# Performance work log

Measured on AMD Instinct MI355X. Metric: run time of the kernel, lower is better.

Reference implementation:

```python
import jax, jax.numpy as jnp
import numpy as np

B, D, CROSS = 16384, 2048, 3

def setup_inputs() -> dict:
    key = jax.random.key(0)
    k1, k2 = jax.random.split(key)
    x = jax.random.normal(k1, (B, D), dtype=jnp.float32)
    # glorot_normal for (d,1) weight ~ std sqrt(2/(d+1))
    W = jax.random.normal(k2, (CROSS, D), dtype=jnp.float32) * np.sqrt(2.0 / (D + 1)).astype(np.float32)
    b = jnp.zeros((CROSS, D), dtype=jnp.float32)
    return {"x": x, "W": W, "b": b}

def reference(x, W, b):
    # Original: xl <- (x0 @ xl^T) @ w_i + b_i + xl  with x0, xl shaped [B,d,1].
    # (x0 xl^T) w == x0 * (xl . w), a scalar per row — mathematically identical,
    # avoiding the wasted [B,d,d] outer product.
    x0 = x
    xl = x
    for i in range(CROSS):
        s = jnp.einsum('bd,d->b', xl, W[i])          # [B] scalar dot per row
        xl = x0 * s[:, None] + b[i][None, :] + xl     # scale + bias + residual
    return xl
```

## Files before the change

### kernel.cpp

```cpp
#include <hip/hip_runtime.h>


constexpr int D_DIM    = 2048;
constexpr int NTHREADS = 256;
constexpr int ROWS     = 2;

__device__ __forceinline__ float dot8(const float4 a0, const float4 a1,
                                      const float4 b0, const float4 b1) {
    return a0.x*b0.x + a0.y*b0.y + a0.z*b0.z + a0.w*b0.w
         + a1.x*b1.x + a1.y*b1.y + a1.z*b1.z + a1.w*b1.w;
}

__global__ __launch_bounds__(NTHREADS)
void cross_network_kernel(const float* __restrict__ x,
                          const float* __restrict__ W,
                          const float* __restrict__ bias,
                          float* __restrict__ out) {
    const int row0 = blockIdx.x * ROWS;
    const int t    = threadIdx.x;
    const int lane = t & 63;
    const int wave = t >> 6;

    const float4* xr0 = reinterpret_cast<const float4*>(x + (size_t)row0 * D_DIM);
    const float4* xr1 = reinterpret_cast<const float4*>(x + (size_t)(row0 + 1) * D_DIM);
    const float4 x0a = xr0[t], x0b = xr0[t + NTHREADS];
    const float4 x1a = xr1[t], x1b = xr1[t + NTHREADS];

    const float4* w0r = reinterpret_cast<const float4*>(W);
    const float4* w1r = reinterpret_cast<const float4*>(W + D_DIM);
    const float4* w2r = reinterpret_cast<const float4*>(W + 2 * D_DIM);
    const float4* b0r = reinterpret_cast<const float4*>(bias);
    const float4* b1r = reinterpret_cast<const float4*>(bias + D_DIM);
    const float4* b2r = reinterpret_cast<const float4*>(bias + 2 * D_DIM);

    float p00, p01, p10, p11, p20, p21, q1, q2;
    float4 bsa, bsb;
    {
        const float4 wa = w0r[t], wb = w0r[t + NTHREADS];
        p00 = dot8(x0a, x0b, wa, wb);
        p01 = dot8(x1a, x1b, wa, wb);
    }
    {
        const float4 wa = w1r[t], wb = w1r[t + NTHREADS];
        p10 = dot8(x0a, x0b, wa, wb);
        p11 = dot8(x1a, x1b, wa, wb);
        bsa = b0r[t]; bsb = b0r[t + NTHREADS];
        q1  = dot8(bsa, bsb, wa, wb);
    }
    {
        const float4 wa = w2r[t], wb = w2r[t + NTHREADS];
        p20 = dot8(x0a, x0b, wa, wb);
        p21 = dot8(x1a, x1b, wa, wb);
        const float4 b1a = b1r[t], b1b = b1r[t + NTHREADS];
        bsa.x += b1a.x; bsa.y += b1a.y; bsa.z += b1a.z; bsa.w += b1a.w;
        bsb.x += b1b.x; bsb.y += b1b.y; bsb.z += b1b.z; bsb.w += b1b.w;
        q2  = dot8(bsa, bsb, wa, wb);
    }

#pragma unroll
    for (int off = 32; off >= 1; off >>= 1) {
        p00 += __shfl_down(p00, off, 64);
        p01 += __shfl_down(p01, off, 64);
        p10 += __shfl_down(p10, off, 64);
        p11 += __shfl_down(p11, off, 64);
        p20 += __shfl_down(p20, off, 64);
        p21 += __shfl_down(p21, off, 64);
        q1  += __shfl_down(q1,  off, 64);
        q2  += __shfl_down(q2,  off, 64);
    }

    __shared__ float sred[8][4];
    if (lane == 0) {
        sred[0][wave] = p00; sred[1][wave] = p01;
        sred[2][wave] = p10; sred[3][wave] = p11;
        sred[4][wave] = p20; sred[5][wave] = p21;
        sred[6][wave] = q1;  sred[7][wave] = q2;
    }
    __syncthreads();

    float d[8];
#pragma unroll
    for (int k = 0; k < 8; ++k)
        d[k] = sred[k][0] + sred[k][1] + sred[k][2] + sred[k][3];
    const float c01 = d[6], c02 = d[7];

    float scale[ROWS];
#pragma unroll
    for (int r = 0; r < ROWS; ++r) {
        const float s0 = d[0 + r];
        const float t1 = 1.0f + s0;
        const float s1 = fmaf(t1, d[2 + r], c01);
        const float t2 = t1 + s1;
        const float s2 = fmaf(t2, d[4 + r], c02);
        scale[r] = t2 + s2;
    }

    {
        const float4 b2a = b2r[t], b2b = b2r[t + NTHREADS];
        bsa.x += b2a.x; bsa.y += b2a.y; bsa.z += b2a.z; bsa.w += b2a.w;
        bsb.x += b2b.x; bsb.y += b2b.y; bsb.z += b2b.z; bsb.w += b2b.w;
    }

    float4* o0 = reinterpret_cast<float4*>(out + (size_t)row0 * D_DIM);
    float4* o1 = reinterpret_cast<float4*>(out + (size_t)(row0 + 1) * D_DIM);
    float4 v;
    v.x = fmaf(x0a.x, scale[0], bsa.x); v.y = fmaf(x0a.y, scale[0], bsa.y);
    v.z = fmaf(x0a.z, scale[0], bsa.z); v.w = fmaf(x0a.w, scale[0], bsa.w);
    o0[t] = v;
    v.x = fmaf(x0b.x, scale[0], bsb.x); v.y = fmaf(x0b.y, scale[0], bsb.y);
    v.z = fmaf(x0b.z, scale[0], bsb.z); v.w = fmaf(x0b.w, scale[0], bsb.w);
    o0[t + NTHREADS] = v;
    v.x = fmaf(x1a.x, scale[1], bsa.x); v.y = fmaf(x1a.y, scale[1], bsa.y);
    v.z = fmaf(x1a.z, scale[1], bsa.z); v.w = fmaf(x1a.w, scale[1], bsa.w);
    o1[t] = v;
    v.x = fmaf(x1b.x, scale[1], bsb.x); v.y = fmaf(x1b.y, scale[1], bsb.y);
    v.z = fmaf(x1b.z, scale[1], bsb.z); v.w = fmaf(x1b.w, scale[1], bsb.w);
    o1[t + NTHREADS] = v;
}

extern "C" void kernel_launch(void* const* d_in, const int* in_sizes, int n_in,
                              void* d_out, int out_size, void* d_ws, size_t ws_size,
                              hipStream_t stream) {
    const float* x    = (const float*)d_in[0];
    const float* W    = (const float*)d_in[1];
    const float* bias = (const float*)d_in[2];
    float* out = (float*)d_out;

    const int B = in_sizes[0] / D_DIM;
    cross_network_kernel<<<B / ROWS, NTHREADS, 0, stream>>>(x, W, bias, out);
}
```

Measured before the change: 43.56 us.

## Process multiple row pairs per block, reusing W and bias sums across rows

Each block now loops over four row pairs, loading W rows and computing the bias-sum vector and bias-W dot constants once, then reusing them from registers and shared memory. This removes redundant W/bias loads and reductions per row pair and cuts the block count. Per-iteration barriers serialize row loads without explicit prefetch, which may reduce memory-level parallelism. A double-buffered shared reduction area and a launch-bounds occupancy hint are added.

```diff
diff --git a/kernel.cpp b/kernel.cpp
--- a/kernel.cpp
+++ b/kernel.cpp
@@ -1,121 +1,146 @@
 #include <hip/hip_runtime.h>
 
 
-constexpr int D_DIM    = 2048;
-constexpr int NTHREADS = 256;
-constexpr int ROWS     = 2;
+constexpr int D_DIM   = 2048;
+constexpr int NT      = 256;
+constexpr int NWAVES  = 4;
+constexpr int NITER   = 4;
+constexpr int ROWS_PB = 2 * NITER;
 
 __device__ __forceinline__ float dot8(const float4 a0, const float4 a1,
                                       const float4 b0, const float4 b1) {
-    return a0.x*b0.x + a0.y*b0.y + a0.z*b0.z + a0.w*b0.w
-         + a1.x*b1.x + a1.y*b1.y + a1.z*b1.z + a1.w*b1.w;
+    float s = a0.x * b0.x;
+    s = fmaf(a0.y, b0.y, s); s = fmaf(a0.z, b0.z, s); s = fmaf(a0.w, b0.w, s);
+    s = fmaf(a1.x, b1.x, s); s = fmaf(a1.y, b1.y, s);
+    s = fmaf(a1.z, b1.z, s); s = fmaf(a1.w, b1.w, s);
+    return s;
 }
 
-__global__ __launch_bounds__(NTHREADS)
+__global__ __launch_bounds__(NT, 8)
 void cross_network_kernel(const float* __restrict__ x,
                           const float* __restrict__ W,
                           const float* __restrict__ bias,
                           float* __restrict__ out) {
-    const int row0 = blockIdx.x * ROWS;
     const int t    = threadIdx.x;
     const int lane = t & 63;
     const int wave = t >> 6;
-
-    const float4* xr0 = reinterpret_cast<const float4*>(x + (size_t)row0 * D_DIM);
-    const float4* xr1 = reinterpret_cast<const float4*>(x + (size_t)(row0 + 1) * D_DIM);
-    const float4 x0a = xr0[t], x0b = xr0[t + NTHREADS];
-    const float4 x1a = xr1[t], x1b = xr1[t + NTHREADS];
+    const int rowBase = blockIdx.x * ROWS_PB;
 
     const float4* w0r = reinterpret_cast<const float4*>(W);
     const float4* w1r = reinterpret_cast<const float4*>(W + D_DIM);
     const float4* w2r = reinterpret_cast<const float4*>(W + 2 * D_DIM);
-    const float4* b0r = reinterpret_cast<const float4*>(bias);
-    const float4* b1r = reinterpret_cast<const float4*>(bias + D_DIM);
-    const float4* b2r = reinterpret_cast<const float4*>(bias + 2 * D_DIM);
+    const float4 w0a = w0r[t], w0b = w0r[t + NT];
+    const float4 w1a = w1r[t], w1b = w1r[t + NT];
+    const float4 w2a = w2r[t], w2b = w2r[t + NT];
 
-    float p00, p01, p10, p11, p20, p21, q1, q2;
-    float4 bsa, bsb;
+    __shared__ float4 sbsum[2 * NT];
+    __shared__ float  sredP[2][NWAVES];
+    __shared__ float  sred[2][6][NWAVES];
+
+    float q1, q2;
     {
-        const float4 wa = w0r[t], wb = w0r[t + NTHREADS];
-        p00 = dot8(x0a, x0b, wa, wb);
-        p01 = dot8(x1a, x1b, wa, wb);
+        const float4* b0r = reinterpret_cast<const float4*>(bias);
+        const float4* b1r = reinterpret_cast<const float4*>(bias + D_DIM);
+        const float4* b2r = reinterpret_cast<const float4*>(bias + 2 * D_DIM);
+        const float4 b0a = b0r[t], b0b = b0r[t + NT];
+        const float4 b1a = b1r[t], b1b = b1r[t + NT];
+        const float4 b2a = b2r[t], b2b = b2r[t + NT];
+        q1 = dot8(b0a, b0b, w1a, w1b);
+        float4 sa, sb;
+        sa.x = b0a.x + b1a.x; sa.y = b0a.y + b1a.y;
+        sa.z = b0a.z + b1a.z; sa.w = b0a.w + b1a.w;
+        sb.x = b0b.x + b1b.x; sb.y = b0b.y + b1b.y;
+        sb.z = b0b.z + b1b.z; sb.w = b0b.w + b1b.w;
+        q2 = dot8(sa, sb, w2a, w2b);
+        sa.x += b2a.x; sa.y += b2a.y; sa.z += b2a.z; sa.w += b2a.w;
+        sb.x += b2b.x; sb.y += b2b.y; sb.z += b2b.z; sb.w += b2b.w;
+        sbsum[t]      = sa;
+        sbsum[t + NT] = sb;
+#pragma unroll
+        for (int off = 32; off >= 1; off >>= 1) {
+            q1 += __shfl_down(q1, off, 64);
+            q2 += __shfl_down(q2, off, 64);
+        }
+        if (lane == 0) { sredP[0][wave] = q1; sredP[1][wave] = q2; }
     }
-    {
-        const float4 wa = w1r[t], wb = w1r[t + NTHREADS];
-        p10 = dot8(x0a, x0b, wa, wb);
-        p11 = dot8(x1a, x1b, wa, wb);
-        bsa = b0r[t]; bsb = b0r[t + NTHREADS];
-        q1  = dot8(bsa, bsb, wa, wb);
-    }
-    {
-        const float4 wa = w2r[t], wb = w2r[t + NTHREADS];
-        p20 = dot8(x0a, x0b, wa, wb);
-        p21 = dot8(x1a, x1b, wa, wb);
-        const float4 b1a = b1r[t], b1b = b1r[t + NTHREADS];
-        bsa.x += b1a.x; bsa.y += b1a.y; bsa.z += b1a.z; bsa.w += b1a.w;
-        bsb.x += b1b.x; bsb.y += b1b.y; bsb.z += b1b.z; bsb.w += b1b.w;
-        q2  = dot8(bsa, bsb, wa, wb);
-    }
+    __syncthreads();
+    const float c01 = sredP[0][0] + sredP[0][1] + sredP[0][2] + sredP[0][3];
+    const float c02 = sredP[1][0] + sredP[1][1] + sredP[1][2] + sredP[1][3];
+
+    for (int it = 0; it < NITER; ++it) {
+        const int row0 = rowBase + 2 * it;
+        const float4* xr0 = reinterpret_cast<const float4*>(x + (size_t)row0 * D_DIM);
+        const float4* xr1 = reinterpret_cast<const float4*>(x + (size_t)(row0 + 1) * D_DIM);
+        const float4 x0a = xr0[t], x0b = xr0[t + NT];
+        const float4 x1a = xr1[t], x1b = xr1[t + NT];
+
+        float p00 = dot8(x0a, x0b, w0a, w0b);
+        float p01 = dot8(x1a, x1b, w0a, w0b);
+        float p10 = dot8(x0a, x0b, w1a, w1b);
+        float p11 = dot8(x1a, x1b, w1a, w1b);
+        float p20 = dot8(x0a, x0b, w2a, w2b);
+        float p21 = dot8(x1a, x1b, w2a, w2b);
 
 #pragma unroll
-    for (int off = 32; off >= 1; off >>= 1) {
-        p00 += __shfl_down(p00, off, 64);
-        p01 += __shfl_down(p01, off, 64);
-        p10 += __shfl_down(p10, off, 64);
-        p11 += __shfl_down(p11, off, 64);
-        p20 += __shfl_down(p20, off, 64);
-        p21 += __shfl_down(p21, off, 64);
-        q1  += __shfl_down(q1,  off, 64);
-        q2  += __shfl_down(q2,  off, 64);
+        for (int off = 32; off >= 1; off >>= 1) {
+            p00 += __shfl_down(p00, off, 64);
+            p01 += __shfl_down(p01, off, 64);
+            p10 += __shfl_down(p10, off, 64);
+            p11 += __shfl_down(p11, off, 64);
+            p20 += __shfl_down(p20, off, 64);
+            p21 += __shfl_down(p21, off, 64);
+        }
+
+        float (*sr)[NWAVES] = sred[it & 1];
+        if (lane == 0) {
+            sr[0][wave] = p00; sr[1][wave] = p01;
+            sr[2][wave] = p10; sr[3][wave] = p11;
+            sr[4][wave] = p20; sr[5][wave] = p21;
+        }
+        __syncthreads();
+
+        const float d00 = sr[0][0] + sr[0][1] + sr[0][2] + sr[0][3];
+        const float d01 = sr[1][0] + sr[1][1] + sr[1][2] + sr[1][3];
+        const float d10 = sr[2][0] + sr[2][1] + sr[2][2] + sr[2][3];
+        const float d11 = sr[3][0] + sr[3][1] + sr[3][2] + sr[3][3];
+        const float d20 = sr[4][0] + sr[4][1] + sr[4][2] + sr[4][3];
+        const float d21 = sr[5][0] + sr[5][1] + sr[5][2] + sr[5][3];
+
+        float scale0, scale1;
+        {
+            const float t1 = 1.0f + d00;
+            const float s1 = fmaf(t1, d10, c01);
+            const float t2 = t1 + s1;
+            const float s2 = fmaf(t2, d20, c02);
+            scale0 = t2 + s2;
+        }
+        {
+            const float t1 = 1.0f + d01;
+            const float s1 = fmaf(t1, d11, c01);
+            const float t2 = t1 + s1;
+            const float s2 = fmaf(t2, d21, c02);
+            scale1 = t2 + s2;
+        }
+
+        const float4 bsa = sbsum[t];
+        const float4 bsb = sbsum[t + NT];
+
+        float4* o0 = reinterpret_cast<float4*>(out + (size_t)row0 * D_DIM);
+        float4* o1 = reinterpret_cast<float4*>(out + (size_t)(row0 + 1) * D_DIM);
+        float4 v;
+        v.x = fmaf(x0a.x, scale0, bsa.x); v.y = fmaf(x0a.y, scale0, bsa.y);
+        v.z = fmaf(x0a.z, scale0, bsa.z); v.w = fmaf(x0a.w, scale0, bsa.w);
+        o0[t] = v;
+        v.x = fmaf(x0b.x, scale0, bsb.x); v.y = fmaf(x0b.y, scale0, bsb.y);
+        v.z = fmaf(x0b.z, scale0, bsb.z); v.w = fmaf(x0b.w, scale0, bsb.w);
+        o0[t + NT] = v;
+        v.x = fmaf(x1a.x, scale1, bsa.x); v.y = fmaf(x1a.y, scale1, bsa.y);
+        v.z = fmaf(x1a.z, scale1, bsa.z); v.w = fmaf(x1a.w, scale1, bsa.w);
+        o1[t] = v;
+        v.x = fmaf(x1b.x, scale1, bsb.x); v.y = fmaf(x1b.y, scale1, bsb.y);
+        v.z = fmaf(x1b.z, scale1, bsb.z); v.w = fmaf(x1b.w, scale1, bsb.w);
+        o1[t + NT] = v;
     }
-
-    __shared__ float sred[8][4];
-    if (lane == 0) {
-        sred[0][wave] = p00; sred[1][wave] = p01;
-        sred[2][wave] = p10; sred[3][wave] = p11;
-        sred[4][wave] = p20; sred[5][wave] = p21;
-        sred[6][wave] = q1;  sred[7][wave] = q2;
-    }
-    __syncthreads();
-
-    float d[8];
-#pragma unroll
-    for (int k = 0; k < 8; ++k)
-        d[k] = sred[k][0] + sred[k][1] + sred[k][2] + sred[k][3];
-    const float c01 = d[6], c02 = d[7];
-
-    float scale[ROWS];
-#pragma unroll
-    for (int r = 0; r < ROWS; ++r) {
-        const float s0 = d[0 + r];
-        const float t1 = 1.0f + s0;
-        const float s1 = fmaf(t1, d[2 + r], c01);
-        const float t2 = t1 + s1;
-        const float s2 = fmaf(t2, d[4 + r], c02);
-        scale[r] = t2 + s2;
-    }
-
-    {
-        const float4 b2a = b2r[t], b2b = b2r[t + NTHREADS];
-        bsa.x += b2a.x; bsa.y += b2a.y; bsa.z += b2a.z; bsa.w += b2a.w;
-        bsb.x += b2b.x; bsb.y += b2b.y; bsb.z += b2b.z; bsb.w += b2b.w;
-    }
-
-    float4* o0 = reinterpret_cast<float4*>(out + (size_t)row0 * D_DIM);
-    float4* o1 = reinterpret_cast<float4*>(out + (size_t)(row0 + 1) * D_DIM);
-    float4 v;
-    v.x = fmaf(x0a.x, scale[0], bsa.x); v.y = fmaf(x0a.y, scale[0], bsa.y);
-    v.z = fmaf(x0a.z, scale[0], bsa.z); v.w = fmaf(x0a.w, scale[0], bsa.w);
-    o0[t] = v;
-    v.x = fmaf(x0b.x, scale[0], bsb.x); v.y = fmaf(x0b.y, scale[0], bsb.y);
-    v.z = fmaf(x0b.z, scale[0], bsb.z); v.w = fmaf(x0b.w, scale[0], bsb.w);
-    o0[t + NTHREADS] = v;
-    v.x = fmaf(x1a.x, scale[1], bsa.x); v.y = fmaf(x1a.y, scale[1], bsa.y);
-    v.z = fmaf(x1a.z, scale[1], bsa.z); v.w = fmaf(x1a.w, scale[1], bsa.w);
-    o1[t] = v;
-    v.x = fmaf(x1b.x, scale[1], bsb.x); v.y = fmaf(x1b.y, scale[1], bsb.y);
-    v.z = fmaf(x1b.z, scale[1], bsb.z); v.w = fmaf(x1b.w, scale[1], bsb.w);
-    o1[t + NTHREADS] = v;
 }
 
 extern "C" void kernel_launch(void* const* d_in, const int* in_sizes, int n_in,
@@ -127,5 +152,6 @@
     float* out = (float*)d_out;
 
     const int B = in_sizes[0] / D_DIM;
-    cross_network_kernel<<<B / ROWS, NTHREADS, 0, stream>>>(x, W, bias, out);
+    const int blocks = B / ROWS_PB;
+    cross_network_kernel<<<blocks, NT, 0, stream>>>(x, W, bias, out);
 }
```

After: 58.40 us. +34.1%, slower.
